# Optimization experiments

Hardware: AMD Instinct MI355X
Metric: run time of the kernel (lower is better)

## Reference

```python
import jax, jax.numpy as jnp
import numpy as np

D = 1024
H = 16
DK = D // H
FF = int(8 / 3 * D)  # 2730
EPS = 1e-6


def setup_inputs() -> dict:
    key = jax.random.key(0)
    ks = jax.random.split(key, 8)
    s = lambda n: 1.0 / np.sqrt(n)
    return {
        "x": jax.random.normal(ks[0], (2, 2048, D), dtype=jnp.float32),
        "w_qkv": jax.random.normal(ks[1], (3 * D, D), dtype=jnp.float32) * s(D),
        "w_o": jax.random.normal(ks[2], (D, D), dtype=jnp.float32) * s(D),
        "n1_w": jnp.ones((D,), dtype=jnp.float32),
        "n2_w": jnp.ones((D,), dtype=jnp.float32),
        "w1": jax.random.normal(ks[3], (FF, D), dtype=jnp.float32) * s(D),
        "w2": jax.random.normal(ks[4], (D, FF), dtype=jnp.float32) * s(FF),
        "w3": jax.random.normal(ks[5], (FF, D), dtype=jnp.float32) * s(D),
    }


def _rmsnorm(x, w):
    return x * jax.lax.rsqrt(jnp.mean(x * x, axis=-1, keepdims=True) + EPS) * w


def _attn(x, w_qkv, w_o):
    B, L, _ = x.shape
    qkv = x @ w_qkv.T                       # [B,L,3D]
    qkv = qkv.reshape(B, L, 3, H, DK)
    q, k, v = qkv[:, :, 0], qkv[:, :, 1], qkv[:, :, 2]   # [B,L,H,DK]
    scores = jnp.einsum("blhd,bmhd->bhlm", q, k) / np.sqrt(DK).astype(np.float32)
    attn = jax.nn.softmax(scores, axis=-1)               # [B,H,L,L]
    out = jnp.einsum("bhlm,bmhd->blhd", attn, v).reshape(B, L, D)
    return out @ w_o.T


def _swiglu(x, w1, w2, w3):
    return (jax.nn.silu(x @ w1.T) * (x @ w3.T)) @ w2.T


def reference(x, w_qkv, w_o, n1_w, n2_w, w1, w2, w3):
    x = x + _attn(_rmsnorm(x, n1_w), w_qkv, w_o)
    return x + _swiglu(_rmsnorm(x, n2_w), w1, w2, w3)
```

## Files before the change

kernel.cpp:

```cpp
#include <hip/hip_runtime.h>
#include <stdint.h>


#define LSEQ   2048
#define DMODEL 1024
#define NHEAD  16
#define NTOK   4096
#define FFR    2730
#define FFP    2816
#define FF2    5632

typedef short  short8  __attribute__((ext_vector_type(8)));
typedef float  floatx4 __attribute__((ext_vector_type(4)));

__device__ __forceinline__ uint16_t f2bf(float f) {
  uint32_t u = __builtin_bit_cast(uint32_t, f);
  u += 0x7FFFu + ((u >> 16) & 1u);
  return (uint16_t)(u >> 16);
}
__device__ __forceinline__ uint32_t cvt_pk_bf16(float a, float b) {
  uint32_t d;
  asm("v_cvt_pk_bf16_f32 %0, %1, %2" : "=v"(d) : "v"(a), "v"(b));
  return d;
}
__device__ __forceinline__ void gl2lds16(const void* g, void* l) {
  __builtin_amdgcn_global_load_lds(
      (const __attribute__((address_space(1))) unsigned int*)g,
      (__attribute__((address_space(3))) unsigned int*)l, 16, 0, 0);
}
template <int N>
__device__ __forceinline__ void vm_wait() {
  if constexpr (N == 0)      asm volatile("s_waitcnt vmcnt(0)" ::: "memory");
  else if constexpr (N == 3) asm volatile("s_waitcnt vmcnt(3)" ::: "memory");
  else if constexpr (N == 4) asm volatile("s_waitcnt vmcnt(4)" ::: "memory");
}

__global__ __launch_bounds__(256) void cvt_all_k(const float* __restrict__ wqkv,
                                                 const float* __restrict__ wo,
                                                 const float* __restrict__ w1,
                                                 const float* __restrict__ w3,
                                                 uint16_t* __restrict__ dst) {
  int g = blockIdx.x;
  int c = threadIdx.x * 4;
  const float* src = nullptr;
  if (g < 3072)       src = wqkv + (size_t)g * 1024;
  else if (g < 4096)  src = wo + (size_t)(g - 3072) * 1024;
  else {
    int r = g - 4096;
    int u = r >> 6, wi = r & 63;
    int srow = u * 32 + (wi & 31);
    if (srow < FFR) src = ((wi < 32) ? w1 : w3) + (size_t)srow * 1024;
  }
  float4 v = src ? *(const float4*)(src + c) : float4{0, 0, 0, 0};
  uint64_t pack =  (uint64_t)f2bf(v.x)        | ((uint64_t)f2bf(v.y) << 16)
                | ((uint64_t)f2bf(v.z) << 32) | ((uint64_t)f2bf(v.w) << 48);
  *(uint64_t*)(dst + (size_t)g * 1024 + c) = pack;
}

__global__ __launch_bounds__(256) void cvt_pad_k(const float* __restrict__ src,
                                                 uint16_t* __restrict__ dst,
                                                 int rows, int cols, int cols_p) {
  long idx = (long)blockIdx.x * 256 + threadIdx.x;
  int c4 = cols_p >> 2;
  if (idx >= (long)rows * c4) return;
  int r = (int)(idx / c4);
  int c = (int)(idx % c4) * 4;
  uint64_t pack;
  if (c + 3 < cols) {
    const float* sp = src + (size_t)r * cols + c;
    float2 a = *(const float2*)sp;
    float2 b2 = *(const float2*)(sp + 2);
    pack =  (uint64_t)f2bf(a.x)        | ((uint64_t)f2bf(a.y) << 16)
         | ((uint64_t)f2bf(b2.x) << 32) | ((uint64_t)f2bf(b2.y) << 48);
  } else {
    pack = 0;
    for (int e = 0; e < 4; e++) {
      float v = (c + e < cols) ? src[(size_t)r * cols + c + e] : 0.0f;
      pack |= (uint64_t)f2bf(v) << (16 * e);
    }
  }
  *(uint64_t*)(dst + (size_t)r * cols_p + c) = pack;
}

__global__ __launch_bounds__(256) void rmsnorm_k(const float* __restrict__ x,
                                                 const float* __restrict__ wgt,
                                                 uint16_t* __restrict__ out) {
  const int row = blockIdx.x;
  const int c = threadIdx.x * 4;
  const float* xr = x + (size_t)row * DMODEL;
  float4 v = *(const float4*)(xr + c);
  float ss = v.x * v.x + v.y * v.y + v.z * v.z + v.w * v.w;
#pragma unroll
  for (int off = 32; off >= 1; off >>= 1) ss += __shfl_down(ss, off, 64);
  __shared__ float red[4];
  if ((threadIdx.x & 63) == 0) red[threadIdx.x >> 6] = ss;
  __syncthreads();
  float tot = red[0] + red[1] + red[2] + red[3];
  float scale = rsqrtf(tot * (1.0f / DMODEL) + 1e-6f);
  float4 wv = *(const float4*)(wgt + c);
  uint64_t pack =  (uint64_t)f2bf(v.x * scale * wv.x)
                | ((uint64_t)f2bf(v.y * scale * wv.y) << 16)
                | ((uint64_t)f2bf(v.z * scale * wv.z) << 32)
                | ((uint64_t)f2bf(v.w * scale * wv.w) << 48);
  *(uint64_t*)(out + (size_t)row * DMODEL + c) = pack;
}

template <int MODE, int TM, int TN>
__global__ __launch_bounds__(256) void gemm_bt(const uint16_t* __restrict__ A,
                                               const uint16_t* __restrict__ B,
                                               uint16_t* __restrict__ Cb,
                                               float* __restrict__ Cf,
                                               const float* __restrict__ Res,
                                               int M, int N, int K) {
  constexpr int FI = TM / 32, FJ = TN / 32;
  constexpr int NIT = (TM + TN) / 64;
  constexpr int BUFO = (TM + TN) * 32;
  __shared__ uint16_t S[2 * BUFO];
  const int tid = threadIdx.x;
  const int w = tid >> 6, lane = tid & 63;
  const int grp = lane >> 4, l16 = lane & 15;
  const int m0 = blockIdx.y * TM, n0 = blockIdx.x * TN;
  const int rw = (w >> 1) * (TM / 2), cw = (w & 1) * (TN / 2);

  floatx4 acc[FI][FJ] = {};

  const uint16_t* gp[NIT];
  uint16_t* lp[NIT];
#pragma unroll
  for (int i = 0; i < NIT; i++) {
    int c = i * 256 + tid;
    if (c < TM * 4) {
      gp[i] = A + (size_t)(m0 + (c >> 2)) * K + (c & 3) * 8;
      lp[i] = S + c * 8;
    } else {
      int c2 = c - TM * 4;
      gp[i] = B + (size_t)(n0 + (c2 >> 2)) * K + (c2 & 3) * 8;
      lp[i] = S + TM * 32 + c2 * 8;
    }
  }

  const int nt = K / 32;

  auto stage = [&](int t, int buf) {
#pragma unroll
    for (int i = 0; i < NIT; i++) gl2lds16(gp[i] + t * 32, lp[i] + buf * BUFO);
  };
  auto compute = [&](int buf) {
    const uint16_t* Sb = S + buf * BUFO;
    short8 af[FI], bfr[FJ];
#pragma unroll
    for (int i = 0; i < FI; i++)
      af[i] = *(const short8*)(Sb + (rw + i * 16 + l16) * 32 + grp * 8);
#pragma unroll
    for (int j = 0; j < FJ; j++)
      bfr[j] = *(const short8*)(Sb + TM * 32 + (cw + j * 16 + l16) * 32 + grp * 8);
#pragma unroll
    for (int i = 0; i < FI; i++)
#pragma unroll
      for (int j = 0; j < FJ; j++)
        acc[i][j] = __builtin_amdgcn_mfma_f32_16x16x32_bf16(af[i], bfr[j], acc[i][j], 0, 0, 0);
  };

  stage(0, 0);
  stage(1, 1);
  __builtin_amdgcn_sched_barrier(0);
  vm_wait<NIT>();
  __builtin_amdgcn_sched_barrier(0);
  __builtin_amdgcn_s_barrier();
  __builtin_amdgcn_sched_barrier(0);

  for (int t = 0;;) {
    compute(0);
    if (++t == nt) break;
    __builtin_amdgcn_s_barrier();
    __builtin_amdgcn_sched_barrier(0);
    if (t + 1 < nt) { stage(t + 1, 0); __builtin_amdgcn_sched_barrier(0); vm_wait<NIT>(); }
    else            vm_wait<0>();
    __builtin_amdgcn_sched_barrier(0);
    __builtin_amdgcn_s_barrier();
    __builtin_amdgcn_sched_barrier(0);

    compute(1);
    if (++t == nt) break;
    __builtin_amdgcn_s_barrier();
    __builtin_amdgcn_sched_barrier(0);
    if (t + 1 < nt) { stage(t + 1, 1); __builtin_amdgcn_sched_barrier(0); vm_wait<NIT>(); }
    else            vm_wait<0>();
    __builtin_amdgcn_sched_barrier(0);
    __builtin_amdgcn_s_barrier();
    __builtin_amdgcn_sched_barrier(0);
  }

  if constexpr (MODE == 2) {
    const int half = N >> 1;
#pragma unroll
    for (int i = 0; i < FI; i++) {
      const int mrow = m0 + rw + i * 16 + grp * 4;
#pragma unroll
      for (int j = 0; j < 2; j++) {
        const int gcol = (n0 >> 1) + (cw >> 1) + j * 16 + l16;
#pragma unroll
        for (int r = 0; r < 4; r++) {
          float a = acc[i][j][r];
          float bv = acc[i][j + 2][r];
          float ex = __builtin_amdgcn_exp2f(-a * 1.4426950408889634f);
          float s = a * __builtin_amdgcn_rcpf(1.0f + ex);
          Cb[(size_t)(mrow + r) * half + gcol] = f2bf(s * bv);
        }
      }
    }
  } else {
#pragma unroll
    for (int i = 0; i < FI; i++) {
#pragma unroll
      for (int j = 0; j < FJ; j++) {
        const int mrow = m0 + rw + i * 16 + grp * 4;
        const int ncol = n0 + cw + j * 16 + l16;
#pragma unroll
        for (int r = 0; r < 4; r++) {
          size_t idx = (size_t)(mrow + r) * N + ncol;
          float v = acc[i][j][r];
          if (MODE == 0) Cb[idx] = f2bf(v);
          else           Cf[idx] = v + Res[idx];
        }
      }
    }
  }
}

__global__ __launch_bounds__(256, 2) void attn_flash(const uint16_t* __restrict__ qkv,
                                                     uint16_t* __restrict__ outp) {
  const int tid = threadIdx.x;
  const int w = tid >> 6, lane = tid & 63;
  const int grp = lane >> 4, l16 = lane & 15;
  const int lin = blockIdx.x;
  const int xcd = lin & 7;
  const int slot = lin >> 3;
  const int pair = xcd * 4 + (slot >> 4);
  const int qc = slot & 15;
  const int h = pair & 15, b = pair >> 4;
  const int q0 = qc * 128;

  __shared__ uint16_t Ks[2][4096];
  __shared__ uint16_t Vt[2][64 * 76];
  __shared__ uint16_t Ps[128 * 76];

  const size_t base = ((size_t)b * LSEQ) * 3072 + (size_t)h * 64;

  short8 aq[2][2];
#pragma unroll
  for (int fi = 0; fi < 2; fi++) {
    const uint16_t* qr = qkv + base + (size_t)(q0 + w * 32 + fi * 16 + l16) * 3072;
    aq[fi][0] = *(const short8*)(qr + grp * 8);
    aq[fi][1] = *(const short8*)(qr + 32 + grp * 8);
  }

#pragma unroll
  for (int i = 0; i < 2; i++) {
    int c = i * 256 + tid;
    int row = c >> 3, cc = (c & 7) ^ (row & 7);
    gl2lds16(qkv + base + (size_t)row * 3072 + 1024 + cc * 8, Ks[0] + c * 8);
  }
#pragma unroll
  for (int i = 0; i < 2; i++) {
    int c = i * 256 + tid;
    int tt = c & 63, db = c >> 6;
    uint4 vv = *(const uint4*)(qkv + base + (size_t)tt * 3072 + 2048 + db * 8);
    uint32_t uu[4] = {vv.x, vv.y, vv.z, vv.w};
#pragma unroll
    for (int e = 0; e < 4; e++) {
      Vt[0][(db * 8 + e * 2 + 0) * 76 + tt] = (uint16_t)(uu[e] & 0xFFFFu);
      Vt[0][(db * 8 + e * 2 + 1) * 76 + tt] = (uint16_t)(uu[e] >> 16);
    }
  }
  __syncthreads();

  float lsum[2] = {};
  floatx4 o_acc[2][4] = {};
  const float C = 0.125f * 1.4426950408889634f;

  for (int kc = 0; kc < LSEQ / 64; kc++) {
    const int cur = kc & 1, nxt = cur ^ 1;
    const bool pre = (kc + 1 < LSEQ / 64);
    const int t1 = (kc + 1) * 64;
    uint4 vv[2];
    if (pre) {
#pragma unroll
      for (int i = 0; i < 2; i++) {
        int c = i * 256 + tid;
        int row = c >> 3, cc = (c & 7) ^ (row & 7);
        gl2lds16(qkv + base + (size_t)(t1 + row) * 3072 + 1024 + cc * 8, Ks[nxt] + c * 8);
      }
#pragma unroll
      for (int i = 0; i < 2; i++) {
        int c = i * 256 + tid;
        int tt = c & 63, db = c >> 6;
        vv[i] = *(const uint4*)(qkv + base + (size_t)(t1 + tt) * 3072 + 2048 + db * 8);
      }
    }

    floatx4 s_acc[4][2] = {};
    __builtin_amdgcn_s_setprio(1);
#pragma unroll
    for (int j = 0; j < 4; j++) {
      const int krow = j * 16 + l16;
#pragma unroll
      for (int kk = 0; kk < 2; kk++) {
        int cc = kk * 4 + grp;
        short8 bk = *(const short8*)(Ks[cur] + (krow * 8 + (cc ^ (krow & 7))) * 8);
#pragma unroll
        for (int fi = 0; fi < 2; fi++)
          s_acc[j][fi] = __builtin_amdgcn_mfma_f32_16x16x32_bf16(bk, aq[fi][kk], s_acc[j][fi], 0, 0, 0);
      }
    }
    __builtin_amdgcn_s_setprio(0);

#pragma unroll
    for (int j = 0; j < 4; j++)
#pragma unroll
      for (int fi = 0; fi < 2; fi++) {
        float p0 = __builtin_amdgcn_exp2f(s_acc[j][fi][0] * C);
        float p1 = __builtin_amdgcn_exp2f(s_acc[j][fi][1] * C);
        float p2 = __builtin_amdgcn_exp2f(s_acc[j][fi][2] * C);
        float p3 = __builtin_amdgcn_exp2f(s_acc[j][fi][3] * C);
        lsum[fi] += (p0 + p1) + (p2 + p3);
        uint2 pk;
        pk.x = cvt_pk_bf16(p0, p1);
        pk.y = cvt_pk_bf16(p2, p3);
        *(uint2*)(Ps + (w * 32 + fi * 16 + l16) * 76 + j * 16 + grp * 4) = pk;
      }

    __builtin_amdgcn_s_setprio(1);
#pragma unroll
    for (int kk = 0; kk < 2; kk++) {
      short8 ap0 = *(const short8*)(Ps + (w * 32 + l16) * 76 + kk * 32 + grp * 8);
      short8 ap1 = *(const short8*)(Ps + (w * 32 + 16 + l16) * 76 + kk * 32 + grp * 8);
#pragma unroll
      for (int jj = 0; jj < 4; jj++) {
        short8 bv = *(const short8*)(Vt[cur] + (jj * 16 + l16) * 76 + kk * 32 + grp * 8);
        o_acc[0][jj] = __builtin_amdgcn_mfma_f32_16x16x32_bf16(ap0, bv, o_acc[0][jj], 0, 0, 0);
        o_acc[1][jj] = __builtin_amdgcn_mfma_f32_16x16x32_bf16(ap1, bv, o_acc[1][jj], 0, 0, 0);
      }
    }
    __builtin_amdgcn_s_setprio(0);

    if (pre) {
#pragma unroll
      for (int i = 0; i < 2; i++) {
        int c = i * 256 + tid;
        int tt = c & 63, db = c >> 6;
        uint32_t uu[4] = {vv[i].x, vv[i].y, vv[i].z, vv[i].w};
#pragma unroll
        for (int e = 0; e < 4; e++) {
          Vt[nxt][(db * 8 + e * 2 + 0) * 76 + tt] = (uint16_t)(uu[e] & 0xFFFFu);
          Vt[nxt][(db * 8 + e * 2 + 1) * 76 + tt] = (uint16_t)(uu[e] >> 16);
        }
      }
    }
    __syncthreads();
  }

#pragma unroll
  for (int fi = 0; fi < 2; fi++) {
    lsum[fi] += __shfl_xor(lsum[fi], 16, 64);
    lsum[fi] += __shfl_xor(lsum[fi], 32, 64);
  }
  float lsr[2][4];
#pragma unroll
  for (int fi = 0; fi < 2; fi++)
#pragma unroll
    for (int r = 0; r < 4; r++)
      lsr[fi][r] = __shfl(lsum[fi], grp * 4 + r, 64);
#pragma unroll
  for (int fi = 0; fi < 2; fi++)
#pragma unroll
    for (int jj = 0; jj < 4; jj++)
#pragma unroll
      for (int r = 0; r < 4; r++) {
        int row = b * LSEQ + q0 + w * 32 + fi * 16 + grp * 4 + r;
        float o = o_acc[fi][jj][r] * __builtin_amdgcn_rcpf(lsr[fi][r]);
        outp[(size_t)row * DMODEL + h * 64 + jj * 16 + l16] = f2bf(o);
      }
}

extern "C" void kernel_launch(void* const* d_in, const int* in_sizes, int n_in,
                              void* d_out, int out_size, void* d_ws, size_t ws_size,
                              hipStream_t stream) {
  const float* x    = (const float*)d_in[0];
  const float* wqkv = (const float*)d_in[1];
  const float* wo   = (const float*)d_in[2];
  const float* n1w  = (const float*)d_in[3];
  const float* n2w  = (const float*)d_in[4];
  const float* w1   = (const float*)d_in[5];
  const float* w2   = (const float*)d_in[6];
  const float* w3   = (const float*)d_in[7];
  float* out = (float*)d_out;

  char* p = (char*)d_ws;
  uint16_t* wall  = (uint16_t*)p; p += (size_t)9728 * 1024 * 2;
  uint16_t* wqkvb = wall;
  uint16_t* wob   = wall + (size_t)3072 * 1024;
  uint16_t* w13b  = wall + (size_t)4096 * 1024;
  uint16_t* w2b   = (uint16_t*)p; p += (size_t)1024 * FFP * 2;
  uint16_t* h1    = (uint16_t*)p; p += (size_t)NTOK * DMODEL * 2;
  uint16_t* qkvb  = (uint16_t*)p; p += (size_t)NTOK * 3072 * 2;
  uint16_t* attno = (uint16_t*)p; p += (size_t)NTOK * DMODEL * 2;
  float*    x1    = (float*)p;    p += (size_t)NTOK * DMODEL * 4;
  uint16_t* h2    = (uint16_t*)p; p += (size_t)NTOK * DMODEL * 2;
  uint16_t* gbuf  = (uint16_t*)p; p += (size_t)NTOK * FFP * 2;

  cvt_all_k<<<9728, 256, 0, stream>>>(wqkv, wo, w1, w3, wall);
  cvt_pad_k<<<(1024 * (FFP / 4)) / 256, 256, 0, stream>>>(w2, w2b, 1024, FFR, FFP);

  rmsnorm_k<<<NTOK, 256, 0, stream>>>(x, n1w, h1);
  gemm_bt<0, 128, 128><<<dim3(3072 / 128, NTOK / 128), 256, 0, stream>>>(
      h1, wqkvb, qkvb, nullptr, nullptr, NTOK, 3072, 1024);
  attn_flash<<<512, 256, 0, stream>>>(qkvb, attno);
  gemm_bt<1, 128, 64><<<dim3(1024 / 64, NTOK / 128), 256, 0, stream>>>(
      attno, wob, nullptr, x1, x, NTOK, 1024, 1024);
  rmsnorm_k<<<NTOK, 256, 0, stream>>>(x1, n2w, h2);
  gemm_bt<2, 128, 128><<<dim3(FF2 / 128, NTOK / 128), 256, 0, stream>>>(
      h2, w13b, gbuf, nullptr, nullptr, NTOK, FF2, 1024);
  gemm_bt<1, 128, 64><<<dim3(1024 / 64, NTOK / 128), 256, 0, stream>>>(
      gbuf, w2b, nullptr, out, x1, NTOK, 1024, FFP);
}
```

Measured before the change: 346.3 us.

## Split attention work across 8 waves with 16 query rows each

The flash attention kernel now runs 512 threads (8 waves) per block instead of 256, and each wave owns 16 query rows instead of 32. Every thread loads one K/V chunk per tile instead of two. The aim is to raise wave-level parallelism and latency hiding and to cut per-thread register pressure. In exchange, each K/V tile loaded into LDS feeds fewer MFMAs per wave, the higher thread count makes barrier synchronisation more costly, and the launch_bounds occupancy hint now asks for two 512-thread blocks per CU.

Measured after the change: 337.9 us. -2.4%, faster.

```diff
diff --git a/kernel.cpp b/kernel.cpp
--- a/kernel.cpp
+++ b/kernel.cpp
@@ -228,7 +228,7 @@
   }
 }
 
-__global__ __launch_bounds__(256, 2) void attn_flash(const uint16_t* __restrict__ qkv,
+__global__ __launch_bounds__(512, 2) void attn_flash(const uint16_t* __restrict__ qkv,
                                                      uint16_t* __restrict__ outp) {
   const int tid = threadIdx.x;
   const int w = tid >> 6, lane = tid & 63;
@@ -247,23 +247,20 @@
 
   const size_t base = ((size_t)b * LSEQ) * 3072 + (size_t)h * 64;
 
-  short8 aq[2][2];
-#pragma unroll
-  for (int fi = 0; fi < 2; fi++) {
-    const uint16_t* qr = qkv + base + (size_t)(q0 + w * 32 + fi * 16 + l16) * 3072;
-    aq[fi][0] = *(const short8*)(qr + grp * 8);
-    aq[fi][1] = *(const short8*)(qr + 32 + grp * 8);
-  }
-
-#pragma unroll
-  for (int i = 0; i < 2; i++) {
-    int c = i * 256 + tid;
+  short8 aq[2];
+  {
+    const uint16_t* qr = qkv + base + (size_t)(q0 + w * 16 + l16) * 3072;
+    aq[0] = *(const short8*)(qr + grp * 8);
+    aq[1] = *(const short8*)(qr + 32 + grp * 8);
+  }
+
+  {
+    int c = tid;
     int row = c >> 3, cc = (c & 7) ^ (row & 7);
     gl2lds16(qkv + base + (size_t)row * 3072 + 1024 + cc * 8, Ks[0] + c * 8);
   }
-#pragma unroll
-  for (int i = 0; i < 2; i++) {
-    int c = i * 256 + tid;
+  {
+    int c = tid;
     int tt = c & 63, db = c >> 6;
     uint4 vv = *(const uint4*)(qkv + base + (size_t)tt * 3072 + 2048 + db * 8);
     uint32_t uu[4] = {vv.x, vv.y, vv.z, vv.w};
@@ -275,31 +272,24 @@
   }
   __syncthreads();
 
-  float lsum[2] = {};
-  floatx4 o_acc[2][4] = {};
+  float lsum = 0.0f;
+  floatx4 o_acc[4] = {};
   const float C = 0.125f * 1.4426950408889634f;
 
   for (int kc = 0; kc < LSEQ / 64; kc++) {
     const int cur = kc & 1, nxt = cur ^ 1;
     const bool pre = (kc + 1 < LSEQ / 64);
     const int t1 = (kc + 1) * 64;
-    uint4 vv[2];
+    uint4 vv;
     if (pre) {
-#pragma unroll
-      for (int i = 0; i < 2; i++) {
-        int c = i * 256 + tid;
-        int row = c >> 3, cc = (c & 7) ^ (row & 7);
-        gl2lds16(qkv + base + (size_t)(t1 + row) * 3072 + 1024 + cc * 8, Ks[nxt] + c * 8);
-      }
-#pragma unroll
-      for (int i = 0; i < 2; i++) {
-        int c = i * 256 + tid;
-        int tt = c & 63, db = c >> 6;
-        vv[i] = *(const uint4*)(qkv + base + (size_t)(t1 + tt) * 3072 + 2048 + db * 8);
-      }
-    }
-
-    floatx4 s_acc[4][2] = {};
+      int c = tid;
+      int row = c >> 3, cc = (c & 7) ^ (row & 7);
+      gl2lds16(qkv + base + (size_t)(t1 + row) * 3072 + 1024 + cc * 8, Ks[nxt] + c * 8);
+      int tt = c & 63, db = c >> 6;
+      vv = *(const uint4*)(qkv + base + (size_t)(t1 + tt) * 3072 + 2048 + db * 8);
+    }
+
+    floatx4 s_acc[4] = {};
     __builtin_amdgcn_s_setprio(1);
 #pragma unroll
     for (int j = 0; j < 4; j++) {
@@ -308,79 +298,62 @@
       for (int kk = 0; kk < 2; kk++) {
         int cc = kk * 4 + grp;
         short8 bk = *(const short8*)(Ks[cur] + (krow * 8 + (cc ^ (krow & 7))) * 8);
-#pragma unroll
-        for (int fi = 0; fi < 2; fi++)
-          s_acc[j][fi] = __builtin_amdgcn_mfma_f32_16x16x32_bf16(bk, aq[fi][kk], s_acc[j][fi], 0, 0, 0);
+        s_acc[j] = __builtin_amdgcn_mfma_f32_16x16x32_bf16(bk, aq[kk], s_acc[j], 0, 0, 0);
       }
     }
     __builtin_amdgcn_s_setprio(0);
 
 #pragma unroll
-    for (int j = 0; j < 4; j++)
-#pragma unroll
-      for (int fi = 0; fi < 2; fi++) {
-        float p0 = __builtin_amdgcn_exp2f(s_acc[j][fi][0] * C);
-        float p1 = __builtin_amdgcn_exp2f(s_acc[j][fi][1] * C);
-        float p2 = __builtin_amdgcn_exp2f(s_acc[j][fi][2] * C);
-        float p3 = __builtin_amdgcn_exp2f(s_acc[j][fi][3] * C);
-        lsum[fi] += (p0 + p1) + (p2 + p3);
-        uint2 pk;
-        pk.x = cvt_pk_bf16(p0, p1);
-        pk.y = cvt_pk_bf16(p2, p3);
-        *(uint2*)(Ps + (w * 32 + fi * 16 + l16) * 76 + j * 16 + grp * 4) = pk;
-      }
+    for (int j = 0; j < 4; j++) {
+      float p0 = __builtin_amdgcn_exp2f(s_acc[j][0] * C);
+      float p1 = __builtin_amdgcn_exp2f(s_acc[j][1] * C);
+      float p2 = __builtin_amdgcn_exp2f(s_acc[j][2] * C);
+      float p3 = __builtin_amdgcn_exp2f(s_acc[j][3] * C);
+      lsum += (p0 + p1) + (p2 + p3);
+      uint2 pk;
+      pk.x = cvt_pk_bf16(p0, p1);
+      pk.y = cvt_pk_bf16(p2, p3);
+      *(uint2*)(Ps + (w * 16 + l16) * 76 + j * 16 + grp * 4) = pk;
+    }
 
     __builtin_amdgcn_s_setprio(1);
 #pragma unroll
     for (int kk = 0; kk < 2; kk++) {
-      short8 ap0 = *(const short8*)(Ps + (w * 32 + l16) * 76 + kk * 32 + grp * 8);
-      short8 ap1 = *(const short8*)(Ps + (w * 32 + 16 + l16) * 76 + kk * 32 + grp * 8);
+      short8 ap = *(const short8*)(Ps + (w * 16 + l16) * 76 + kk * 32 + grp * 8);
 #pragma unroll
       for (int jj = 0; jj < 4; jj++) {
         short8 bv = *(const short8*)(Vt[cur] + (jj * 16 + l16) * 76 + kk * 32 + grp * 8);
-        o_acc[0][jj] = __builtin_amdgcn_mfma_f32_16x16x32_bf16(ap0, bv, o_acc[0][jj], 0, 0, 0);
-        o_acc[1][jj] = __builtin_amdgcn_mfma_f32_16x16x32_bf16(ap1, bv, o_acc[1][jj], 0, 0, 0);
+        o_acc[jj] = __builtin_amdgcn_mfma_f32_16x16x32_bf16(ap, bv, o_acc[jj], 0, 0, 0);
       }
     }
     __builtin_amdgcn_s_setprio(0);
 
     if (pre) {
-#pragma unroll
-      for (int i = 0; i < 2; i++) {
-        int c = i * 256 + tid;
-        int tt = c & 63, db = c >> 6;
-        uint32_t uu[4] = {vv[i].x, vv[i].y, vv[i].z, vv[i].w};
-#pragma unroll
-        for (int e = 0; e < 4; e++) {
-          Vt[nxt][(db * 8 + e * 2 + 0) * 76 + tt] = (uint16_t)(uu[e] & 0xFFFFu);
-          Vt[nxt][(db * 8 + e * 2 + 1) * 76 + tt] = (uint16_t)(uu[e] >> 16);
-        }
+      int c = tid;
+      int tt = c & 63, db = c >> 6;
+      uint32_t uu[4] = {vv.x, vv.y, vv.z, vv.w};
+#pragma unroll
+      for (int e = 0; e < 4; e++) {
+        Vt[nxt][(db * 8 + e * 2 + 0) * 76 + tt] = (uint16_t)(uu[e] & 0xFFFFu);
+        Vt[nxt][(db * 8 + e * 2 + 1) * 76 + tt] = (uint16_t)(uu[e] >> 16);
       }
     }
     __syncthreads();
   }
 
-#pragma unroll
-  for (int fi = 0; fi < 2; fi++) {
-    lsum[fi] += __shfl_xor(lsum[fi], 16, 64);
-    lsum[fi] += __shfl_xor(lsum[fi], 32, 64);
-  }
-  float lsr[2][4];
-#pragma unroll
-  for (int fi = 0; fi < 2; fi++)
-#pragma unroll
-    for (int r = 0; r < 4; r++)
-      lsr[fi][r] = __shfl(lsum[fi], grp * 4 + r, 64);
-#pragma unroll
-  for (int fi = 0; fi < 2; fi++)
-#pragma unroll
-    for (int jj = 0; jj < 4; jj++)
-#pragma unroll
-      for (int r = 0; r < 4; r++) {
-        int row = b * LSEQ + q0 + w * 32 + fi * 16 + grp * 4 + r;
-        float o = o_acc[fi][jj][r] * __builtin_amdgcn_rcpf(lsr[fi][r]);
-        outp[(size_t)row * DMODEL + h * 64 + jj * 16 + l16] = f2bf(o);
-      }
+  lsum += __shfl_xor(lsum, 16, 64);
+  lsum += __shfl_xor(lsum, 32, 64);
+  float lsr[4];
+#pragma unroll
+  for (int r = 0; r < 4; r++) lsr[r] = __shfl(lsum, grp * 4 + r, 64);
+#pragma unroll
+  for (int jj = 0; jj < 4; jj++)
+#pragma unroll
+    for (int r = 0; r < 4; r++) {
+      int row = b * LSEQ + q0 + w * 16 + grp * 4 + r;
+      float o = o_acc[jj][r] * __builtin_amdgcn_rcpf(lsr[r]);
+      outp[(size_t)row * DMODEL + h * 64 + jj * 16 + l16] = f2bf(o);
+    }
 }
 
 extern "C" void kernel_launch(void* const* d_in, const int* in_sizes, int n_in,
@@ -415,7 +388,7 @@
   rmsnorm_k<<<NTOK, 256, 0, stream>>>(x, n1w, h1);
   gemm_bt<0, 128, 128><<<dim3(3072 / 128, NTOK / 128), 256, 0, stream>>>(
       h1, wqkvb, qkvb, nullptr, nullptr, NTOK, 3072, 1024);
-  attn_flash<<<512, 256, 0, stream>>>(qkvb, attno);
+  attn_flash<<<512, 512, 0, stream>>>(qkvb, attno);
   gemm_bt<1, 128, 64><<<dim3(1024 / 64, NTOK / 128), 256, 0, stream>>>(
       attno, wob, nullptr, x1, x, NTOK, 1024, 1024);
   rmsnorm_k<<<NTOK, 256, 0, stream>>>(x1, n2w, h2);
```
